# Performance work log

Hardware: AMD Instinct MI355X
Metric: run time of the kernel (lower is better)

Reference implementation:

```python
import jax, jax.numpy as jnp
import numpy as np

EPS = 0.01  # added to std devs per the docstring to avoid div by zero


def _patches(A, p, H_out, W_out):
    # A: padded [B, D, Hp, Wp] -> [B, D, H_out, W_out, p*p] 5x5 neighborhoods
    return jnp.stack([A[:, :, u:u + H_out, v:v + W_out]
                      for u in range(p) for v in range(p)], axis=-1)


def _normalize(P):
    mu = P.mean(axis=-1, keepdims=True)
    sd = P.std(axis=-1, keepdims=True)  # population std over the p*p patch
    return (P - mu) / (sd + EPS)


def setup_inputs() -> dict:
    key = jax.random.key(0)
    k1, k2 = jax.random.split(key)
    B, D, H, W = 16, 64, 48, 24
    X = jax.random.normal(k1, (B, D, H, W), dtype=jnp.float32)
    Y = jax.random.normal(k2, (B, D, H, W), dtype=jnp.float32)
    return {"X": X, "Y": Y, "patch_size": 5}


def reference(X, Y, patch_size):
    B, D, H, W = X.shape
    p = patch_size
    d = p // 2
    n = p * p
    # X padded d on all sides; Y gets extra vertical padding (2*d) so patches
    # centered at rows x-d .. x+d are valid for every x.
    Xp = jnp.pad(X, ((0, 0), (0, 0), (d, d), (d, d)))
    Yp = jnp.pad(Y, ((0, 0), (0, 0), (2 * d, 2 * d), (d, d)))
    En = _normalize(_patches(Xp, p, H, W))             # [B,D,H,W,n]
    Fn = _normalize(_patches(Yp, p, H + 2 * d, W))     # [B,D,H+2d,W,n]
    # vertical search offsets a-d in [-d, d]: Fs[a] holds Y patches at row x+a-d
    Fs = jnp.stack([Fn[:, :, a:a + H] for a in range(2 * d + 1)], axis=0)  # [p,B,D,H,W,n]
    # ncc(E,F) = mean_k En_k * Fn_k ; output channel order: depth i, then
    # vertical offset a, then Y column c (out_depth = p * W * D)
    out = jnp.einsum('bdxyk,abdxck->bdacxy', En, Fs) / n  # [B,D,p,W,H,W]
    return out.reshape(B, D * p * W, H, W)
```

## Files before the change

### kernel.cpp

```cpp
#include <hip/hip_runtime.h>


#define BH 48
#define BW 24
constexpr float EPS = 0.01f;

#define XPS 29
#define YTS 57
#define IVS 53

__global__ __launch_bounds__(192, 3) void ncc_kernel(const float* __restrict__ X,
                                                     const float* __restrict__ Y,
                                                     float* __restrict__ out) {
    __shared__ float Xp[52 * XPS];
    __shared__ float YpT[28 * YTS];
    __shared__ float invYT[24 * IVS];

    const int bd  = blockIdx.x;
    const int tid = threadIdx.x;

    const float* Xg = X + (size_t)bd * (BH * BW);
    const float* Yg = Y + (size_t)bd * (BH * BW);

    for (int i = tid; i < 52 * 28; i += 192) {
        int r = i / 28, c = i % 28;
        int orr = r - 2, oc = c - 2;
        float v = 0.f;
        if (orr >= 0 && orr < BH && oc >= 0 && oc < BW) v = Xg[orr * BW + oc];
        Xp[r * XPS + c] = v;
    }
    for (int i = tid; i < 56 * 28; i += 192) {
        int r = i / 28, c = i % 28;
        int orr = r - 4, oc = c - 2;
        float v = 0.f;
        if (orr >= 0 && orr < BH && oc >= 0 && oc < BW) v = Yg[orr * BW + oc];
        YpT[c * YTS + r] = v;
    }
    __syncthreads();

    for (int i = tid; i < 52 * 24; i += 192) {
        int c = i % 24, r = i / 24;
        float s = 0.f, s2 = 0.f;
#pragma unroll
        for (int v = 0; v < 5; ++v)
#pragma unroll
            for (int u = 0; u < 5; ++u) {
                float val = YpT[(c + v) * YTS + (r + u)];
                s += val;
                s2 += val * val;
            }
        float mu  = s * 0.04f;
        float var = fmaxf(s2 * 0.04f - mu * mu, 0.f);
        invYT[c * IVS + r] = 1.f / (sqrtf(var) + EPS);
    }
    __syncthreads();

    const int y  = tid % 24;
    const int xs = tid / 24;
    float* ob0 = out + (size_t)bd * (5 * 24 * 48 * 24);

#pragma unroll 1
    for (int xi = 0; xi < 6; ++xi) {
        const int x = xi * 8 + xs;

        float xn[25];
        float s = 0.f, s2 = 0.f;
#pragma unroll
        for (int u = 0; u < 5; ++u)
#pragma unroll
            for (int v = 0; v < 5; ++v) {
                float val = Xp[(x + u) * XPS + (y + v)];
                xn[u * 5 + v] = val;
                s += val;
                s2 += val * val;
            }
        float mu  = s * 0.04f;
        float var = fmaxf(s2 * 0.04f - mu * mu, 0.f);
        float sc  = 0.04f / (sqrtf(var) + EPS);
#pragma unroll
        for (int k = 0; k < 25; ++k) xn[k] = (xn[k] - mu) * sc;

        float* ob = ob0 + x * 24 + y;

        float w[5][9];
#pragma unroll
        for (int v = 0; v < 5; ++v)
#pragma unroll
            for (int r = 0; r < 9; ++r)
                w[v][r] = YpT[v * YTS + x + r];

#pragma unroll
        for (int c = 0; c < 24; ++c) {
            float dot[5] = {0.f, 0.f, 0.f, 0.f, 0.f};
#pragma unroll
            for (int u = 0; u < 5; ++u)
#pragma unroll
                for (int v = 0; v < 5; ++v) {
                    const float f  = xn[u * 5 + v];
                    const int  sl  = (c + v) % 5;
#pragma unroll
                    for (int a = 0; a < 5; ++a)
                        dot[a] += f * w[sl][a + u];
                }
#pragma unroll
            for (int a = 0; a < 5; ++a) {
                float iv = invYT[c * IVS + (x + a)];
                ob[(size_t)(a * 24 + c) * (48 * 24)] = dot[a] * iv;
            }
            if (c < 23) {
#pragma unroll
                for (int r = 0; r < 9; ++r)
                    w[c % 5][r] = YpT[(c + 5) * YTS + x + r];
            }
        }
    }
}

extern "C" void kernel_launch(void* const* d_in, const int* in_sizes, int n_in,
                              void* d_out, int out_size, void* d_ws, size_t ws_size,
                              hipStream_t stream) {
    const float* X = (const float*)d_in[0];
    const float* Y = (const float*)d_in[1];
    float* out = (float*)d_out;
    ncc_kernel<<<dim3(1024), dim3(192), 0, stream>>>(X, Y, out);
}
```

Baseline: 618.4 us.

## Remap threads to one row and three columns each, loop over vertical offset

The block grows from 192 to 384 threads. Each thread now owns one output row x and three adjacent output columns, so it keeps three normalized X patches in registers, and the outer loop runs over the vertical offset a instead of six row iterations. Each Y weight value is reused across three X patches rather than across five offsets. The three consecutive float stores per thread make the global writes more contiguous. In exchange, register pressure from holding 75 patch values may cost occupancy, and the same Y patches are reloaded from shared memory for every offset.

```diff
diff --git a/kernel.cpp b/kernel.cpp
--- a/kernel.cpp
+++ b/kernel.cpp
@@ -9,7 +9,7 @@
 #define YTS 57
 #define IVS 53
 
-__global__ __launch_bounds__(192, 3) void ncc_kernel(const float* __restrict__ X,
+__global__ __launch_bounds__(384, 4) void ncc_kernel(const float* __restrict__ X,
                                                      const float* __restrict__ Y,
                                                      float* __restrict__ out) {
     __shared__ float Xp[52 * XPS];
@@ -22,14 +22,14 @@
     const float* Xg = X + (size_t)bd * (BH * BW);
     const float* Yg = Y + (size_t)bd * (BH * BW);
 
-    for (int i = tid; i < 52 * 28; i += 192) {
+    for (int i = tid; i < 52 * 28; i += 384) {
         int r = i / 28, c = i % 28;
         int orr = r - 2, oc = c - 2;
         float v = 0.f;
         if (orr >= 0 && orr < BH && oc >= 0 && oc < BW) v = Xg[orr * BW + oc];
         Xp[r * XPS + c] = v;
     }
-    for (int i = tid; i < 56 * 28; i += 192) {
+    for (int i = tid; i < 56 * 28; i += 384) {
         int r = i / 28, c = i % 28;
         int orr = r - 4, oc = c - 2;
         float v = 0.f;
@@ -38,7 +38,7 @@
     }
     __syncthreads();
 
-    for (int i = tid; i < 52 * 24; i += 192) {
+    for (int i = tid; i < 52 * 24; i += 384) {
         int c = i % 24, r = i / 24;
         float s = 0.f, s2 = 0.f;
 #pragma unroll
@@ -55,22 +55,19 @@
     }
     __syncthreads();
 
-    const int y  = tid % 24;
-    const int xs = tid / 24;
-    float* ob0 = out + (size_t)bd * (5 * 24 * 48 * 24);
+    const int x  = tid >> 3;
+    const int y0 = (tid & 7) * 3;
 
-#pragma unroll 1
-    for (int xi = 0; xi < 6; ++xi) {
-        const int x = xi * 8 + xs;
-
-        float xn[25];
+    float xn[3][25];
+#pragma unroll
+    for (int j = 0; j < 3; ++j) {
         float s = 0.f, s2 = 0.f;
 #pragma unroll
         for (int u = 0; u < 5; ++u)
 #pragma unroll
             for (int v = 0; v < 5; ++v) {
-                float val = Xp[(x + u) * XPS + (y + v)];
-                xn[u * 5 + v] = val;
+                float val = Xp[(x + u) * XPS + (y0 + j + v)];
+                xn[j][u * 5 + v] = val;
                 s += val;
                 s2 += val * val;
             }
@@ -78,39 +75,43 @@
         float var = fmaxf(s2 * 0.04f - mu * mu, 0.f);
         float sc  = 0.04f / (sqrtf(var) + EPS);
 #pragma unroll
-        for (int k = 0; k < 25; ++k) xn[k] = (xn[k] - mu) * sc;
+        for (int k = 0; k < 25; ++k) xn[j][k] = (xn[j][k] - mu) * sc;
+    }
 
-        float* ob = ob0 + x * 24 + y;
+    float* op = out + (size_t)bd * (5 * 24 * 48 * 24) + 3 * tid;
 
-        float w[5][9];
+#pragma unroll 1
+    for (int a = 0; a < 5; ++a) {
+        const int yr = x + a;
+
+        float w[5][5];
 #pragma unroll
         for (int v = 0; v < 5; ++v)
 #pragma unroll
-            for (int r = 0; r < 9; ++r)
-                w[v][r] = YpT[v * YTS + x + r];
+            for (int u = 0; u < 5; ++u)
+                w[v][u] = YpT[v * YTS + (yr + u)];
 
 #pragma unroll
         for (int c = 0; c < 24; ++c) {
-            float dot[5] = {0.f, 0.f, 0.f, 0.f, 0.f};
+            float d0 = 0.f, d1 = 0.f, d2 = 0.f;
 #pragma unroll
             for (int u = 0; u < 5; ++u)
 #pragma unroll
                 for (int v = 0; v < 5; ++v) {
-                    const float f  = xn[u * 5 + v];
-                    const int  sl  = (c + v) % 5;
-#pragma unroll
-                    for (int a = 0; a < 5; ++a)
-                        dot[a] += f * w[sl][a + u];
+                    const float f = w[(c + v) % 5][u];
+                    d0 += xn[0][u * 5 + v] * f;
+                    d1 += xn[1][u * 5 + v] * f;
+                    d2 += xn[2][u * 5 + v] * f;
                 }
-#pragma unroll
-            for (int a = 0; a < 5; ++a) {
-                float iv = invYT[c * IVS + (x + a)];
-                ob[(size_t)(a * 24 + c) * (48 * 24)] = dot[a] * iv;
-            }
+            const float iv = invYT[c * IVS + yr];
+            op[0] = d0 * iv;
+            op[1] = d1 * iv;
+            op[2] = d2 * iv;
+            op += 48 * 24;
             if (c < 23) {
 #pragma unroll
-                for (int r = 0; r < 9; ++r)
-                    w[c % 5][r] = YpT[(c + 5) * YTS + x + r];
+                for (int u = 0; u < 5; ++u)
+                    w[c % 5][u] = YpT[(c + 5) * YTS + (yr + u)];
             }
         }
     }
@@ -122,5 +123,5 @@
     const float* X = (const float*)d_in[0];
     const float* Y = (const float*)d_in[1];
     float* out = (float*)d_out;
-    ncc_kernel<<<dim3(1024), dim3(192), 0, stream>>>(X, Y, out);
+    ncc_kernel<<<dim3(1024), dim3(384), 0, stream>>>(X, Y, out);
 }
```

Measured after the change: 594.2 us. 3.9% less time.
